# Kernel optimization log

Hardware: AMD Instinct MI355X
Metric: run time of the kernel (lower is better)

## Reference

```python
import jax, jax.numpy as jnp
import numpy as np

# Hyperparameters matching init_kwargs
DIM = 1024
HEADS = 16
MEM_HIDDEN = 512
FF_DIM = 4096
CHUNK = 128
NPERSIST = 16
ALPHA = 0.02
THETA = 0.1
ETA = 0.9
B, T = 2, 1024


def _mem_read(x, p):
    """DeepMemory forward: 2-layer MLP dim->hidden->dim with SiLU between."""
    W1, b1, W2, b2 = p
    h = jax.nn.silu(x @ W1.T + b1)
    return h @ W2.T + b2


def setup_inputs() -> dict:
    key = jax.random.key(0)
    ks = jax.random.split(key, 16)
    s = 0.02  # weight init scale
    return {
        "x": jax.random.normal(ks[0], (B, T, DIM), jnp.float32),
        "Wqkv": jax.random.normal(ks[1], (3 * DIM, DIM), jnp.float32) * s,
        "mW1": jax.random.normal(ks[2], (MEM_HIDDEN, DIM), jnp.float32) * s,
        "mb1": jnp.zeros((MEM_HIDDEN,), jnp.float32),
        "mW2": jax.random.normal(ks[3], (DIM, MEM_HIDDEN), jnp.float32) * s,
        "mb2": jnp.zeros((DIM,), jnp.float32),
        "P": jax.random.normal(ks[4], (1, NPERSIST, DIM), jnp.float32),
        "Wqkv_attn": jax.random.normal(ks[5], (3 * DIM, DIM), jnp.float32) * s,
        "Wo": jax.random.normal(ks[6], (DIM, DIM), jnp.float32) * s,
        "ffW1": jax.random.normal(ks[7], (FF_DIM, DIM), jnp.float32) * s,
        "ffb1": jnp.zeros((FF_DIM,), jnp.float32),
        "ffW2": jax.random.normal(ks[8], (DIM, FF_DIM), jnp.float32) * s,
        "ffb2": jnp.zeros((DIM,), jnp.float32),
    }


def reference(x, Wqkv, mW1, mb1, mW2, mb2, P, Wqkv_attn, Wo, ffW1, ffb1, ffW2, ffb2):
    Bb, Tt, D = x.shape
    nC = Tt // CHUNK

    # shared qkv projection (bias-free Linear)
    qkv = x @ Wqkv.T                       # [B,T,3D]
    K = qkv[..., D:2 * D]
    V = qkv[..., 2 * D:]

    # chunked test-time memory writes: k,v are detached in the torch code
    Kc = jax.lax.stop_gradient(K).reshape(Bb, nC, CHUNK, D).transpose(1, 0, 2, 3)  # [nC,B,C,D]
    Vc = jax.lax.stop_gradient(V).reshape(Bb, nC, CHUNK, D).transpose(1, 0, 2, 3)

    params0 = tuple(jax.lax.stop_gradient(p) for p in (mW1, mb1, mW2, mb2))
    mom0 = tuple(jnp.zeros_like(p) for p in params0)

    def loss_fn(p, k, v):
        return jnp.mean((_mem_read(k, p) - v) ** 2)

    def step(carry, kv):
        p, m = carry
        k, v = kv
        g = jax.grad(loss_fn)(p, k, v)
        # momentum: s = eta*s - theta*g ; weight: w = (1-alpha)*w + s
        m = tuple(ETA * mi - THETA * gi for mi, gi in zip(m, g))
        p = tuple((1.0 - ALPHA) * pi + mi for pi, mi in zip(p, m))
        return (p, m), None

    (pf, _), _ = jax.lax.scan(step, (params0, mom0), (Kc, Vc))
    pf = jax.lax.stop_gradient(pf)  # fast weights are buffers (non-differentiable)

    # memory readout tokens for the whole segment
    Q = qkv[..., :D]
    mem_tok = _mem_read(Q, pf)             # [B,T,D]

    # concatenate persistent + memory + input tokens
    tokens = jnp.concatenate([jnp.broadcast_to(P, (Bb, NPERSIST, D)), mem_tok, x], axis=1)
    N = tokens.shape[1]                    # NPERSIST + 2T
    dh = D // HEADS

    # causal multi-head attention over the concatenated sequence
    aqkv = tokens @ Wqkv_attn.T            # [B,N,3D]
    q, k, v = jnp.split(aqkv, 3, axis=-1)
    to_heads = lambda t: t.reshape(Bb, N, HEADS, dh).transpose(0, 2, 1, 3)
    q, k, v = to_heads(q), to_heads(k), to_heads(v)
    scores = jnp.einsum('bhnd,bhmd->bhnm', q, k) / jnp.sqrt(jnp.float32(dh))
    causal = jnp.tril(jnp.ones((N, N), bool))
    scores = jnp.where(causal, scores, jnp.float32(-1e9))
    attn = jax.nn.softmax(scores, axis=-1)
    o = jnp.einsum('bhnm,bhmd->bhnd', attn, v).transpose(0, 2, 1, 3).reshape(Bb, N, D)
    y = o @ Wo.T

    # feed-forward (no residual in source)
    y = jax.nn.gelu(y @ ffW1.T + ffb1) @ ffW2.T + ffb2

    # drop persistent + memory tokens, gate by a fresh memory read
    out = y[:, NPERSIST + Tt:, :]          # [B,T,D]
    newQ = (out @ Wqkv.T)[..., :D]
    return out * _mem_read(newQ, pf)
```

## Files before the change

kernel.cpp:

```cpp
#include <hip/hip_runtime.h>
#include <math.h>

#define BATCH 2
#define TSEQ 1024
#define DIMD 1024
#define NPERS 16
#define NCH 8
#define NTOK 2064
#define ETA_C 0.9f
#define THETA_C 0.1f
#define ALPHA_C 0.02f

typedef __attribute__((ext_vector_type(4))) float f32x4;
typedef __attribute__((ext_vector_type(8))) short s16x8;
typedef unsigned short u16;

__device__ __forceinline__ u16 f2bf(float f) {
    unsigned int u = __float_as_uint(f);
    return (u16)((u + 0x7fffu + ((u >> 16) & 1u)) >> 16);
}
__device__ __forceinline__ float bf2f(u16 h) { return __uint_as_float(((unsigned)h) << 16); }
__device__ __forceinline__ void split2(float v, u16& h, u16& l) {
    h = f2bf(v); l = f2bf(v - bf2f(h));
}

static const size_t oRA = 0;
static const size_t oRB = 50724864;
static const size_t oRC = 67633152;
static const size_t oRD = 80216064;
static const size_t oRE = 96993280;
static const size_t oRF = 109576192;
static const size_t oRG = 113770496;
static const size_t oRH = 117970944;

static const size_t PW1 = 0, PB1 = 524288, PW2 = 524800, PB2 = 1049088, PSZ = 1050112;

__device__ __forceinline__ void gload_lds16(const u16* g, u16* l) {
    __builtin_amdgcn_global_load_lds(
        (const __attribute__((address_space(1))) unsigned int*)g,
        (__attribute__((address_space(3))) unsigned int*)l, 16, 0, 0);
}

__device__ __forceinline__ void xcd_swizzle(int& bx, int& by) {
    int gx = gridDim.x, nwg = gx * gridDim.y;
    int lid = blockIdx.y * gx + blockIdx.x;
    int t = lid;
    if ((nwg & 7) == 0) {
        int q = nwg >> 3;
        t = (lid & 7) * q + (lid >> 3);
    }
    bx = t % gx; by = t / gx;
}

__device__ __forceinline__ void stage_tile(const u16* sp, u16* buf, int rbase,
                                           int M, int clampM, int K, int k0,
                                           int wid, int lane) {
    const int lr = lane >> 2, lc = lane & 3;
    #pragma unroll
    for (int i = 0; i < 8; ++i) {
        int r = i * 16 + lr;
        int gr = rbase + r;
        if (clampM && gr >= M) gr = M - 1;
        int g = lc ^ ((r >> 1) & 3);
        gload_lds16(sp + (size_t)gr * K + k0 + g * 8, buf + wid * 4096 + i * 512);
    }
}

__device__ __forceinline__ void stage_tile64(const u16* sp, u16* buf, int rbase,
                                             int K, int k0, int wid, int lane) {
    const int lr = lane >> 3, lc = lane & 7;
    #pragma unroll
    for (int i = 0; i < 16; ++i) {
        int r = i * 8 + lr;
        int gr = rbase + r;
        int g = lc ^ (r & 7);
        gload_lds16(sp + (size_t)gr * K + k0 + g * 8, buf + wid * 8192 + i * 512);
    }
}

template<int NPROD>
__device__ __forceinline__ void mm_loop32(u16 lds[2][16384],
                const u16* sp, int rbase, int M, int clampM, int K,
                int kbeg, int kend, int wid, int lane, int wm, int wn,
                f32x4 acc[4][4]) {
    const int frow = lane & 15, kblk = lane >> 4;
    const int nt = (kend - kbeg) >> 5;
    const int doStage = (NPROD == 3) || (wid != 1);
    if (doStage) stage_tile(sp, lds[0], rbase, M, clampM, K, kbeg, wid, lane);
    for (int t = 0; t < nt; ++t) {
        __syncthreads();
        if (t + 1 < nt && doStage)
            stage_tile(sp, lds[(t + 1) & 1], rbase, M, clampM, K, kbeg + ((t + 1) << 5), wid, lane);
        const u16* cb = lds[t & 1];
        s16x8 bh[4], bl[4];
        #pragma unroll
        for (int ni = 0; ni < 4; ++ni) {
            int br = wn * 64 + ni * 16 + frow;
            int pc = kblk ^ ((br >> 1) & 3);
            bh[ni] = *(const s16x8*)&cb[2 * 4096 + br * 32 + pc * 8];
            bl[ni] = *(const s16x8*)&cb[3 * 4096 + br * 32 + pc * 8];
        }
        #pragma unroll
        for (int mi = 0; mi < 4; ++mi) {
            int ar = wm * 64 + mi * 16 + frow;
            int pc = kblk ^ ((ar >> 1) & 3);
            s16x8 ah = *(const s16x8*)&cb[0 * 4096 + ar * 32 + pc * 8];
            s16x8 al;
            if (NPROD == 3) al = *(const s16x8*)&cb[1 * 4096 + ar * 32 + pc * 8];
            #pragma unroll
            for (int ni = 0; ni < 4; ++ni) {
                acc[mi][ni] = __builtin_amdgcn_mfma_f32_16x16x32_bf16(ah, bh[ni], acc[mi][ni], 0, 0, 0);
                acc[mi][ni] = __builtin_amdgcn_mfma_f32_16x16x32_bf16(ah, bl[ni], acc[mi][ni], 0, 0, 0);
                if (NPROD == 3)
                    acc[mi][ni] = __builtin_amdgcn_mfma_f32_16x16x32_bf16(al, bh[ni], acc[mi][ni], 0, 0, 0);
            }
        }
    }
}

template<int ACTF, int WF32, int WSPLIT, int PARTIAL, int NPROD>
__global__ __launch_bounds__(256)
void gemm_mfma_k(const u16* __restrict__ Ah, const u16* __restrict__ Al,
                 const u16* __restrict__ Wh, const u16* __restrict__ Wl,
                 float* __restrict__ C, u16* __restrict__ Chi, u16* __restrict__ Clo,
                 int M, int N, int K, const float* __restrict__ bias)
{
    __shared__ u16 lds[2][16384];
    const int tid = threadIdx.x;
    const int lane = tid & 63, wid = tid >> 6;
    const int wm = wid >> 1, wn = wid & 1;
    int bx, by; xcd_swizzle(bx, by);
    const int row0 = by * 128, col0 = bx * 128;
    const u16* sp = (wid == 0) ? Ah : (wid == 1) ? Al : (wid == 2) ? Wh : Wl;
    const int rbase = (wid < 2) ? row0 : col0;
    const int clampM = (wid < 2) ? 1 : 0;
    f32x4 acc[4][4] = {};
    int kbeg = 0, kend = K;
    if (PARTIAL) {
        int Kseg = K / gridDim.z;
        kbeg = blockIdx.z * Kseg;
        kend = kbeg + Kseg;
    }
    mm_loop32<NPROD>(lds, sp, rbase, M, clampM, K, kbeg, kend, wid, lane, wm, wn, acc);

    const int erow = (lane >> 4) * 4, ecol = lane & 15;
    #pragma unroll
    for (int mi = 0; mi < 4; ++mi) {
        #pragma unroll
        for (int ni = 0; ni < 4; ++ni) {
            int c = col0 + wn * 64 + ni * 16 + ecol;
            float bv = (!PARTIAL && bias) ? bias[c] : 0.f;
            #pragma unroll
            for (int reg = 0; reg < 4; ++reg) {
                int r = row0 + wm * 64 + mi * 16 + erow + reg;
                if (r >= M) continue;
                float v = acc[mi][ni][reg] + bv;
                if (PARTIAL) {
                    C[((size_t)blockIdx.z * M + r) * N + c] = v;
                    continue;
                }
                if (ACTF == 1) v = v / (1.f + __expf(-v));
                else if (ACTF == 2) {
                    float u = 0.7978845608028654f * (v + 0.044715f * v * v * v);
                    v = 0.5f * v * (1.f + tanhf(u));
                }
                size_t o = (size_t)r * N + c;
                if (WF32) C[o] = v;
                if (WSPLIT) { u16 h, l; split2(v, h, l); Chi[o] = h; Clo[o] = l; }
            }
        }
    }
}

__global__ __launch_bounds__(256)
void gemm_qkv_k(const u16* __restrict__ Ah, const u16* __restrict__ Al,
                const u16* __restrict__ Wh, const u16* __restrict__ Wl,
                u16* __restrict__ Qh, u16* __restrict__ Ql,
                u16* __restrict__ kch, u16* __restrict__ kcl,
                u16* __restrict__ kcTh, u16* __restrict__ kcTl,
                float* __restrict__ Vb, int M, int N, int K)
{
    __shared__ u16 lds[2][16384];
    const int tid = threadIdx.x;
    const int lane = tid & 63, wid = tid >> 6;
    const int wm = wid >> 1, wn = wid & 1;
    int bx, by; xcd_swizzle(bx, by);
    const int row0 = by * 128, col0 = bx * 128;
    const u16* sp = (wid == 0) ? Ah : (wid == 1) ? Al : (wid == 2) ? Wh : Wl;
    const int rbase = (wid < 2) ? row0 : col0;
    f32x4 acc[4][4] = {};
    mm_loop32<3>(lds, sp, rbase, M, 0, K, 0, K, wid, lane, wm, wn, acc);

    const int erow = (lane >> 4) * 4, ecol = lane & 15;
    #pragma unroll
    for (int mi = 0; mi < 4; ++mi) {
        #pragma unroll
        for (int ni = 0; ni < 4; ++ni) {
            int c = col0 + wn * 64 + ni * 16 + ecol;
            #pragma unroll
            for (int reg = 0; reg < 4; ++reg) {
                int r = row0 + wm * 64 + mi * 16 + erow + reg;
                float v = acc[mi][ni][reg];
                int b = r >> 10, t = r & 1023;
                if (c < 1024) {
                    size_t o = (size_t)r * 1024 + c;
                    u16 h, l; split2(v, h, l); Qh[o] = h; Ql[o] = l;
                } else if (c < 2048) {
                    int d = c - 1024;
                    int ch = t >> 7, rr = t & 127;
                    size_t o = ((size_t)((ch * 2 + b) * 128 + rr)) * 1024 + d;
                    u16 h, l; split2(v, h, l);
                    kch[o] = h; kcl[o] = l;
                    size_t ot = (size_t)ch * 262144 + (size_t)d * 256 + b * 128 + rr;
                    kcTh[ot] = h; kcTl[ot] = l;
                } else {
                    int d = c - 2048;
                    int ch = t >> 7, rr = t & 127;
                    Vb[((size_t)((ch * 2 + b) * 128 + rr)) * 1024 + d] = v;
                }
            }
        }
    }
}

__global__ __launch_bounds__(256)
void gemm_aqkv_k(const u16* __restrict__ Ah, const u16* __restrict__ Al,
                 const u16* __restrict__ Wh, const u16* __restrict__ Wl,
                 u16* __restrict__ fQh, u16* __restrict__ fQl,
                 u16* __restrict__ fKh, u16* __restrict__ fKl,
                 u16* __restrict__ fVt, int M, int N, int K)
{
    __shared__ u16 lds[2][16384];
    const int tid = threadIdx.x;
    const int lane = tid & 63, wid = tid >> 6;
    const int wm = wid >> 1, wn = wid & 1;
    int bx, by; xcd_swizzle(bx, by);
    if (bx < 8 && ((by <= 7) || (by >= 17 && by <= 23))) return;
    const int row0 = by * 128, col0 = bx * 128;
    const u16* sp = (wid == 0) ? Ah : (wid == 1) ? Al : (wid == 2) ? Wh : Wl;
    const int rbase = (wid < 2) ? row0 : col0;
    const int clampM = (wid < 2) ? 1 : 0;
    f32x4 acc[4][4] = {};
    mm_loop32<2>(lds, sp, rbase, M, clampM, K, 0, K, wid, lane, wm, wn, acc);

    const int erow = (lane >> 4) * 4, ecol = lane & 15;
    #pragma unroll
    for (int mi = 0; mi < 4; ++mi) {
        #pragma unroll
        for (int ni = 0; ni < 4; ++ni) {
            int c = col0 + wn * 64 + ni * 16 + ecol;
            #pragma unroll
            for (int reg = 0; reg < 4; ++reg) {
                int r = row0 + wm * 64 + mi * 16 + erow + reg;
                if (r >= M) continue;
                float v = acc[mi][ni][reg];
                int b = (r >= 2064) ? 1 : 0;
                int n = r - b * 2064;
                if (c < 1024) {
                    if (n >= NPERS + TSEQ) {
                        int h = c >> 6, d = c & 63;
                        int row = n - (NPERS + TSEQ);
                        size_t o = (((size_t)(b * 16 + h)) * 1024 + row) * 64 + d;
                        u16 hh, ll; split2(0.125f * v, hh, ll);
                        fQh[o] = hh; fQl[o] = ll;
                    }
                } else if (c < 2048) {
                    int cc = c - 1024;
                    int h = cc >> 6, d = cc & 63;
                    size_t o = (((size_t)(b * 16 + h)) * NTOK + n) * 64 + d;
                    u16 hh, ll; split2(v, hh, ll);
                    fKh[o] = hh; fKl[o] = ll;
                } else {
                    int cc = c - 2048;
                    int h = cc >> 6, d = cc & 63;
                    fVt[(((size_t)(b * 16 + h)) * 64 + d) * NTOK + n] = f2bf(v);
                }
            }
        }
    }
}

template<int ACTF, int WF32, int WSPLIT>
__global__ __launch_bounds__(256)
void reduce_k(const float* __restrict__ Cp, int S,
              float* __restrict__ C, u16* __restrict__ Chi, u16* __restrict__ Clo,
              const float* __restrict__ bias, int M, int N)
{
    int i = blockIdx.x * 256 + threadIdx.x;
    int n4 = (int)((size_t)M * N / 4);
    if (i >= n4) return;
    size_t off = (size_t)i * 4;
    float4 v = *(const float4*)&Cp[off];
    for (int z = 1; z < S; ++z) {
        float4 u = *(const float4*)&Cp[(size_t)z * M * N + off];
        v.x += u.x; v.y += u.y; v.z += u.z; v.w += u.w;
    }
    int c = (int)(off % N);
    float vv[4] = {v.x, v.y, v.z, v.w};
    #pragma unroll
    for (int j = 0; j < 4; ++j) {
        float w = vv[j];
        if (bias) w += bias[c + j];
        if (ACTF == 1) w = w / (1.f + __expf(-w));
        else if (ACTF == 2) {
            float u = 0.7978845608028654f * (w + 0.044715f * w * w * w);
            w = 0.5f * w * (1.f + tanhf(u));
        }
        if (WF32) C[off + j] = w;
        if (WSPLIT) { u16 h, l; split2(w, h, l); Chi[off + j] = h; Clo[off + j] = l; }
    }
}

__global__ __launch_bounds__(256)
void reduce_tok_k(const float* __restrict__ Cp, const float* __restrict__ bias,
                  u16* __restrict__ th, u16* __restrict__ tl)
{
    int i = blockIdx.x * 256 + threadIdx.x;
    if (i >= 524288) return;
    size_t off = (size_t)i * 4;
    float4 v = *(const float4*)&Cp[off];
    float4 u = *(const float4*)&Cp[2097152 + off];
    v.x += u.x; v.y += u.y; v.z += u.z; v.w += u.w;
    int r = (int)(off >> 10), c = (int)(off & 1023);
    int b = r >> 10, t = r & 1023;
    size_t orow = (((size_t)(b * NTOK + NPERS + t)) << 10) + c;
    float vv[4] = {v.x + bias[c], v.y + bias[c + 1], v.z + bias[c + 2], v.w + bias[c + 3]};
    u16 h0,l0,h1,l1,h2,l2,h3,l3;
    split2(vv[0],h0,l0); split2(vv[1],h1,l1); split2(vv[2],h2,l2); split2(vv[3],h3,l3);
    ushort4 hv = {h0,h1,h2,h3}, lv = {l0,l1,l2,l3};
    *(ushort4*)&th[orow] = hv;
    *(ushort4*)&tl[orow] = lv;
}

static void gemm_mfma(hipStream_t s, int act, int wf32, int wsplit,
                      const u16* Ah, const u16* Al, const u16* Wh, const u16* Wl,
                      float* C, u16* Ch, u16* Cl, int M, int N, int K,
                      const float* bias, int nprod = 3)
{
    dim3 g(N / 128, (M + 127) / 128), b(256);
    if (act == 0 && wf32 == 1 && wsplit == 0)
        gemm_mfma_k<0,1,0,0,3><<<g,b,0,s>>>(Ah,Al,Wh,Wl,C,Ch,Cl,M,N,K,bias);
    else if (act == 0 && wf32 == 1 && wsplit == 1)
        gemm_mfma_k<0,1,1,0,3><<<g,b,0,s>>>(Ah,Al,Wh,Wl,C,Ch,Cl,M,N,K,bias);
    else if (act == 0 && wf32 == 0 && wsplit == 1)
        gemm_mfma_k<0,0,1,0,3><<<g,b,0,s>>>(Ah,Al,Wh,Wl,C,Ch,Cl,M,N,K,bias);
    else if (act == 1)
        gemm_mfma_k<1,0,1,0,3><<<g,b,0,s>>>(Ah,Al,Wh,Wl,C,Ch,Cl,M,N,K,bias);
    else if (nprod == 2)
        gemm_mfma_k<2,0,1,0,2><<<g,b,0,s>>>(Ah,Al,Wh,Wl,C,Ch,Cl,M,N,K,bias);
    else
        gemm_mfma_k<2,0,1,0,3><<<g,b,0,s>>>(Ah,Al,Wh,Wl,C,Ch,Cl,M,N,K,bias);
}

static void gemm_mfma_sk(hipStream_t s, int act, int wf32, int wsplit,
                         const u16* Ah, const u16* Al, const u16* Wh, const u16* Wl,
                         float* C, u16* Ch, u16* Cl, int M, int N, int K,
                         const float* bias, int S, float* part, int nprod = 3)
{
    if (S <= 1) { gemm_mfma(s, act, wf32, wsplit, Ah, Al, Wh, Wl, C, Ch, Cl, M, N, K, bias, nprod); return; }
    dim3 g(N / 128, (M + 127) / 128, S), b(256);
    if (nprod == 2)
        gemm_mfma_k<0,0,0,1,2><<<g,b,0,s>>>(Ah,Al,Wh,Wl,part,nullptr,nullptr,M,N,K,nullptr);
    else
        gemm_mfma_k<0,0,0,1,3><<<g,b,0,s>>>(Ah,Al,Wh,Wl,part,nullptr,nullptr,M,N,K,nullptr);
    int n4 = (int)((size_t)M * N / 4);
    dim3 rg((n4 + 255) / 256), rb(256);
    if (act == 0 && wf32 == 1 && wsplit == 0)
        reduce_k<0,1,0><<<rg,rb,0,s>>>(part, S, C, Ch, Cl, bias, M, N);
    else if (act == 0 && wf32 == 1 && wsplit == 1)
        reduce_k<0,1,1><<<rg,rb,0,s>>>(part, S, C, Ch, Cl, bias, M, N);
    else if (act == 0 && wf32 == 0 && wsplit == 1)
        reduce_k<0,0,1><<<rg,rb,0,s>>>(part, S, C, Ch, Cl, bias, M, N);
    else if (act == 1)
        reduce_k<1,0,1><<<rg,rb,0,s>>>(part, S, C, Ch, Cl, bias, M, N);
    else
        reduce_k<2,0,1><<<rg,rb,0,s>>>(part, S, C, Ch, Cl, bias, M, N);
}

template<int MODE>
__device__ __forceinline__ void scan_body(u16* lds, int bx, int by,
                 const u16* __restrict__ Ah, const u16* __restrict__ Al,
                 const u16* __restrict__ Wh, const u16* __restrict__ Wl,
                 float* __restrict__ C, u16* __restrict__ Chi, u16* __restrict__ Clo,
                 u16* __restrict__ ChiT, u16* __restrict__ CloT,
                 const float* __restrict__ Zf, const float* __restrict__ add,
                 const float* __restrict__ bias, float* __restrict__ CP,
                 int M, int N, int K, float alpha)
{
    const int tid = threadIdx.x;
    const int lane = tid & 63, wid = tid >> 6;
    const int wm = wid >> 1, wn = wid & 1;
    const int row0 = by * 128, col0 = bx * 128;

    const u16* sp = (wid == 0) ? Ah : (wid == 1) ? Al : (wid == 2) ? Wh : Wl;
    const int rbase = (wid < 2) ? row0 : col0;

    f32x4 acc[4][4] = {};
    const int frow = lane & 15, kblk = lane >> 4;
    const int nt = K >> 6;

    stage_tile64(sp, lds, rbase, K, 0, wid, lane);

    for (int t = 0; t < nt; ++t) {
        __syncthreads();
        if (t + 1 < nt)
            stage_tile64(sp, lds + (((t + 1) & 1) << 15), rbase, K, (t + 1) << 6, wid, lane);
        const u16* cb = lds + ((t & 1) << 15);

        #pragma unroll
        for (int s = 0; s < 2; ++s) {
            s16x8 bh[4], bl[4];
            #pragma unroll
            for (int ni = 0; ni < 4; ++ni) {
                int br = wn * 64 + ni * 16 + frow;
                int pc = (s * 4 + kblk) ^ (br & 7);
                bh[ni] = *(const s16x8*)&cb[2 * 8192 + br * 64 + pc * 8];
                bl[ni] = *(const s16x8*)&cb[3 * 8192 + br * 64 + pc * 8];
            }
            #pragma unroll
            for (int mi = 0; mi < 4; ++mi) {
                int ar = wm * 64 + mi * 16 + frow;
                int pc = (s * 4 + kblk) ^ (ar & 7);
                s16x8 ah = *(const s16x8*)&cb[0 * 8192 + ar * 64 + pc * 8];
                s16x8 al = *(const s16x8*)&cb[1 * 8192 + ar * 64 + pc * 8];
                #pragma unroll
                for (int ni = 0; ni < 4; ++ni) {
                    acc[mi][ni] = __builtin_amdgcn_mfma_f32_16x16x32_bf16(ah, bh[ni], acc[mi][ni], 0, 0, 0);
                    acc[mi][ni] = __builtin_amdgcn_mfma_f32_16x16x32_bf16(ah, bl[ni], acc[mi][ni], 0, 0, 0);
                    acc[mi][ni] = __builtin_amdgcn_mfma_f32_16x16x32_bf16(al, bh[ni], acc[mi][ni], 0, 0, 0);
                }
            }
        }
    }

    const int erow = (lane >> 4) * 4, ecol = lane & 15;
    float csum[4] = {0.f, 0.f, 0.f, 0.f};
    #pragma unroll
    for (int mi = 0; mi < 4; ++mi) {
        #pragma unroll
        for (int ni = 0; ni < 4; ++ni) {
            int c = col0 + wn * 64 + ni * 16 + ecol;
            #pragma unroll
            for (int reg = 0; reg < 4; ++reg) {
                int r = row0 + wm * 64 + mi * 16 + erow + reg;
                float v = acc[mi][ni][reg];
                size_t o = (size_t)r * N + c;
                if (MODE == 1) {
                    v += bias[c];
                    C[o] = v;
                    float hv = v / (1.f + __expf(-v));
                    u16 h, l; split2(hv, h, l);
                    Chi[o] = h; Clo[o] = l;
                    size_t ot = (size_t)c * M + r;
                    ChiT[ot] = h; CloT[ot] = l;
                } else if (MODE == 2) {
                    v += bias[c] - add[o];
                    u16 h, l; split2(v, h, l);
                    Chi[o] = h; Clo[o] = l;
                    size_t ot = (size_t)c * M + r;
                    ChiT[ot] = h; CloT[ot] = l;
                    csum[ni] += v;
                } else if (MODE == 3) {
                    C[o] = alpha * v;
                } else {
                    v *= alpha;
                    float z = Zf[o];
                    float sg = 1.f / (1.f + __expf(-z));
                    v *= sg * (1.f + z * (1.f - sg));
                    u16 h, l; split2(v, h, l);
                    size_t ot = (size_t)c * M + r;
                    ChiT[ot] = h; CloT[ot] = l;
                    csum[ni] += v;
                }
            }
        }
    }
    if (MODE == 2 || MODE == 4) {
        #pragma unroll
        for (int ni = 0; ni < 4; ++ni) {
            float s = csum[ni];
            s += __shfl_xor(s, 16);
            s += __shfl_xor(s, 32);
            if ((lane >> 4) == 0) {
                int c = col0 + wn * 64 + ni * 16 + ecol;
                float w = (MODE == 2) ? alpha * s : s;
                CP[(size_t)(by * 2 + wm) * N + c] = w;
            }
        }
    }
}

template<int MODE>
__global__ __launch_bounds__(256)
void gemm_scan_k(const u16* __restrict__ Ah, const u16* __restrict__ Al,
                 const u16* __restrict__ Wh, const u16* __restrict__ Wl,
                 float* __restrict__ C, u16* __restrict__ Chi, u16* __restrict__ Clo,
                 u16* __restrict__ ChiT, u16* __restrict__ CloT,
                 const float* __restrict__ Zf, const float* __restrict__ add,
                 const float* __restrict__ bias, float* __restrict__ CP,
                 int M, int N, int K, float alpha)
{
    __shared__ u16 lds[2][32768];
    int bx, by; xcd_swizzle(bx, by);
    scan_body<MODE>(&lds[0][0], bx, by, Ah, Al, Wh, Wl, C, Chi, Clo, ChiT, CloT,
                    Zf, add, bias, CP, M, N, K, alpha);
}

__global__ __launch_bounds__(256)
void gemm_scan_pair_k(const u16* __restrict__ rTh, const u16* __restrict__ rTl,
                      const u16* __restrict__ hTh, const u16* __restrict__ hTl,
                      float* __restrict__ gW2,
                      const u16* __restrict__ rh_, const u16* __restrict__ rl_,
                      const u16* __restrict__ w2th, const u16* __restrict__ w2tl,
                      u16* __restrict__ dhTh, u16* __restrict__ dhTl,
                      const float* __restrict__ z1, float* __restrict__ cp1, float cs)
{
    __shared__ u16 lds[2][32768];
    if (blockIdx.y < 8) {
        scan_body<3>(&lds[0][0], blockIdx.x, blockIdx.y, rTh, rTl, hTh, hTl,
                     gW2, nullptr, nullptr, nullptr, nullptr, nullptr, nullptr,
                     nullptr, nullptr, 1024, 512, 256, cs);
    } else {
        scan_body<4>(&lds[0][0], blockIdx.x, blockIdx.y - 8, rh_, rl_, w2th, w2tl,
                     nullptr, nullptr, nullptr, dhTh, dhTl, z1, nullptr,
                     nullptr, cp1, 256, 512, 1024, cs);
    }
}

__global__ void cvt_split_k(const float* __restrict__ in, u16* __restrict__ hi,
                            u16* __restrict__ lo, int n4) {
    int i = blockIdx.x * 256 + threadIdx.x;
    if (i >= n4) return;
    float4 v = *(const float4*)&in[(size_t)i * 4];
    u16 h0,l0,h1,l1,h2,l2,h3,l3;
    split2(v.x,h0,l0); split2(v.y,h1,l1); split2(v.z,h2,l2); split2(v.w,h3,l3);
    ushort4 hv = {h0,h1,h2,h3}, lv = {l0,l1,l2,l3};
    *(ushort4*)&hi[(size_t)i * 4] = hv;
    *(ushort4*)&lo[(size_t)i * 4] = lv;
}
__global__ void transpose_split_k(const float* __restrict__ in, u16* __restrict__ outh,
                                  u16* __restrict__ outl, int R, int C) {
    __shared__ float t[32][33];
    const int c0 = blockIdx.x * 32, r0 = blockIdx.y * 32;
    const size_t zoff = (size_t)blockIdx.z * R * C;
    const int tx = threadIdx.x & 31, ty = threadIdx.x >> 5;
    #pragma unroll
    for (int p = 0; p < 4; ++p) {
        int r = ty + p * 8;
        t[r][tx] = in[zoff + (size_t)(r0 + r) * C + c0 + tx];
    }
    __syncthreads();
    #pragma unroll
    for (int p = 0; p < 4; ++p) {
        int cc = ty + p * 8;
        float v = t[tx][cc];
        u16 h, l; split2(v, h, l);
        size_t o = zoff + (size_t)(c0 + cc) * R + r0 + tx;
        outh[o] = h; outl[o] = l;
    }
}
__global__ void update3_k(float* __restrict__ p, float* __restrict__ mo,
                          const float* __restrict__ g,
                          const float* __restrict__ cp1, const float* __restrict__ cp2,
                          u16* __restrict__ w1h, u16* __restrict__ w1l,
                          u16* __restrict__ w2h, u16* __restrict__ w2l,
                          u16* __restrict__ w2th, u16* __restrict__ w2tl, int n) {
    int i = blockIdx.x * 256 + threadIdx.x;
    if (i >= n) return;
    float gi;
    if (i < 524288) gi = g[i];
    else if (i < 524800) {
        int j = i - 524288;
        gi = cp1[j] + cp1[512 + j] + cp1[1024 + j] + cp1[1536 + j];
    } else if (i < 1049088) gi = g[i];
    else {
        int j = i - 1049088;
        gi = cp2[j] + cp2[1024 + j] + cp2[2048 + j] + cp2[3072 + j];
    }
    float m = ETA_C * mo[i] - THETA_C * gi;
    mo[i] = m;
    float pv = (1.f - ALPHA_C) * p[i] + m;
    p[i] = pv;
    if (i < 524288) {
        u16 h, l; split2(pv, h, l); w1h[i] = h; w1l[i] = l;
    } else if (i >= 524800 && i < 1049088) {
        int j = i - 524800;
        u16 h, l; split2(pv, h, l);
        w2h[j] = h; w2l[j] = l;
        int tj = (j & 511) * 1024 + (j >> 9);
        w2th[tj] = h; w2tl[tj] = l;
    }
}
__global__ void tokens_px_k(const float* __restrict__ P, const float* __restrict__ x,
                            u16* __restrict__ th, u16* __restrict__ tl) {
    size_t idx = (size_t)blockIdx.x * 256 + threadIdx.x;
    if (idx >= (size_t)2 * 1040 * 1024) return;
    int d = (int)(idx & 1023);
    int rl = (int)((idx >> 10) % 1040);
    int b = (int)(idx / ((size_t)1040 * 1024));
    float v; int n;
    if (rl < NPERS) { v = P[(size_t)rl * 1024 + d]; n = rl; }
    else { int t = rl - NPERS; v = x[((size_t)b * TSEQ + t) * 1024 + d]; n = NPERS + TSEQ + t; }
    size_t o = (((size_t)(b * NTOK + n)) << 10) + d;
    u16 h, l; split2(v, h, l); th[o] = h; tl[o] = l;
}
__global__ void mul_k(const float* __restrict__ a, const float* __restrict__ b,
                      float* __restrict__ o, int n) {
    int i = blockIdx.x * 256 + threadIdx.x;
    if (i < n) o[i] = a[i] * b[i];
}

__global__ __launch_bounds__(256)
void flash_part_k(const u16* __restrict__ Qsh, const u16* __restrict__ Qsl,
                  const u16* __restrict__ Ksh, const u16* __restrict__ Ksl,
                  const u16* __restrict__ Vts, float* __restrict__ Of,
                  float* __restrict__ Lf)
{
    __shared__ u16 lds[20480];
    u16* KH = lds;            u16* KL = lds + 4096;
    u16* VT = lds + 8192;
    u16* PH = lds + 12288;    u16* PL = lds + 16384;

    int lid = blockIdx.x + (blockIdx.y << 4) + (blockIdx.z << 8);
    int t1024 = ((lid & 7) << 7) | (lid >> 3);
    const int qt = t1024 & 15, h = (t1024 >> 4) & 15;
    const int zb = t1024 >> 8;
    const int b = zb >> 1, z = zb & 1;

    const int tid = threadIdx.x;
    const int lane = tid & 63, wid = tid >> 6;
    const int fr = lane & 15, kq = lane >> 4;
    const int bh = b * 16 + h;
    const int q0c = qt * 64;
    const int q0a = NPERS + TSEQ + q0c;
    const int ntile = ((q0a + 63) >> 6) + 1;
    const int half = ntile >> 1;
    const int jt0 = z ? half : 0;
    const int jt1 = z ? ntile : half;
    const int l8 = lane & 7, lr8 = lane >> 3;

    auto stageKV = [&](int jt) {
        const int j0 = jt * 64;
        #pragma unroll
        for (int jj = 0; jj < 6; ++jj) {
            int j = wid * 6 + jj;
            int buf = j >> 3, i8 = j & 7;
            if (buf < 2) {
                int row = i8 * 8 + lr8;
                int grow = j0 + row; if (grow > NTOK - 1) grow = NTOK - 1;
                int c = l8 ^ (row & 7);
                const u16* src = (buf == 0 ? Ksh : Ksl) +
                                 (((size_t)bh * NTOK + grow) << 6) + c * 8;
                gload_lds16(src, (buf == 0 ? KH : KL) + i8 * 512);
            } else {
                int d = i8 * 8 + lr8;
                int c = l8 ^ (d & 7);
                int col = j0 + c * 8; if (col > NTOK - 8) col = NTOK - 8;
                const u16* src = Vts + ((size_t)bh * 64 + d) * NTOK + col;
                gload_lds16(src, VT + i8 * 512);
            }
        }
    };

    s16x8 qh[2], ql[2];
    {
        const size_t qrow = ((size_t)bh * 1024 + q0c + wid * 16 + fr) << 6;
        #pragma unroll
        for (int kb = 0; kb < 2; ++kb) {
            qh[kb] = *(const s16x8*)&Qsh[qrow + (size_t)(kb * 4 + kq) * 8];
            ql[kb] = *(const s16x8*)&Qsl[qrow + (size_t)(kb * 4 + kq) * 8];
        }
    }

    f32x4 Oa[4] = {};
    float lrow[4] = {0.f, 0.f, 0.f, 0.f};

    for (int jt = jt0; jt < jt1; ++jt) {
        const int j0 = jt * 64;
        stageKV(jt);
        __syncthreads();

        f32x4 sacc[4] = {};
        __builtin_amdgcn_s_setprio(1);
        #pragma unroll
        for (int nt = 0; nt < 4; ++nt) {
            #pragma unroll
            for (int kb = 0; kb < 2; ++kb) {
                int br = nt * 16 + fr;
                int sl = (kb * 4 + kq) ^ (fr & 7);
                s16x8 kh = *(const s16x8*)&KH[br * 64 + sl * 8];
                s16x8 kl = *(const s16x8*)&KL[br * 64 + sl * 8];
                sacc[nt] = __builtin_amdgcn_mfma_f32_16x16x32_bf16(qh[kb], kh, sacc[nt], 0, 0, 0);
                sacc[nt] = __builtin_amdgcn_mfma_f32_16x16x32_bf16(ql[kb], kh, sacc[nt], 0, 0, 0);
                sacc[nt] = __builtin_amdgcn_mfma_f32_16x16x32_bf16(qh[kb], kl, sacc[nt], 0, 0, 0);
            }
        }
        __builtin_amdgcn_s_setprio(0);

        #pragma unroll
        for (int r = 0; r < 4; ++r) {
            const int qloc = kq * 4 + r;
            const int qi = q0a + wid * 16 + qloc;
            float p4[4], psum = 0.f;
            #pragma unroll
            for (int nt = 0; nt < 4; ++nt) {
                int kj = j0 + nt * 16 + fr;
                float e = (kj <= qi) ? __expf(sacc[nt][r]) : 0.f;
                p4[nt] = e; psum += e;
            }
            #pragma unroll
            for (int off = 1; off < 16; off <<= 1)
                psum += __shfl_xor(psum, off);
            lrow[r] += psum;
            const int prow = wid * 16 + qloc;
            #pragma unroll
            for (int nt = 0; nt < 4; ++nt) {
                u16 ph, pl; split2(p4[nt], ph, pl);
                int col = nt * 16 + fr;
                int sl = (col >> 3) ^ (qloc & 7);
                int off = prow * 64 + sl * 8 + (col & 7);
                PH[off] = ph; PL[off] = pl;
            }
        }

        __builtin_amdgcn_s_setprio(1);
        #pragma unroll
        for (int kb = 0; kb < 2; ++kb) {
            int pr = wid * 16 + fr;
            int sl = (kb * 4 + kq) ^ (fr & 7);
            s16x8 pa = *(const s16x8*)&PH[pr * 64 + sl * 8];
            s16x8 pb = *(const s16x8*)&PL[pr * 64 + sl * 8];
            #pragma unroll
            for (int dt = 0; dt < 4; ++dt) {
                int vr = dt * 16 + fr;
                s16x8 vb = *(const s16x8*)&VT[vr * 64 + sl * 8];
                Oa[dt] = __builtin_amdgcn_mfma_f32_16x16x32_bf16(pa, vb, Oa[dt], 0, 0, 0);
                Oa[dt] = __builtin_amdgcn_mfma_f32_16x16x32_bf16(pb, vb, Oa[dt], 0, 0, 0);
            }
        }
        __builtin_amdgcn_s_setprio(0);
        __syncthreads();
    }

    const size_t obase = ((((size_t)z * 2 + b) * 16 + h) * 16 + qt) * 4096;
    const size_t mlb   = ((((size_t)z * 2 + b) * 16 + h) * 16 + qt) * 64;
    #pragma unroll
    for (int r = 0; r < 4; ++r) {
        int rl = wid * 16 + kq * 4 + r;
        if (fr == 0) Lf[mlb + rl] = lrow[r];
        #pragma unroll
        for (int dt = 0; dt < 4; ++dt)
            Of[obase + (size_t)rl * 64 + dt * 16 + fr] = Oa[dt][r];
    }
}

__global__ __launch_bounds__(256)
void flash_merge_k(const float* __restrict__ Of, const float* __restrict__ Lf,
                   u16* __restrict__ oh, u16* __restrict__ ol)
{
    const int qt = blockIdx.x, h = blockIdx.y, b = blockIdx.z;
    const int tid = threadIdx.x;
    const int row = tid >> 2, quad = tid & 3;
    const size_t b0 = ((((size_t)0 * 2 + b) * 16 + h) * 16 + qt) * 4096 + (size_t)row * 64;
    const size_t b1 = ((((size_t)1 * 2 + b) * 16 + h) * 16 + qt) * 4096 + (size_t)row * 64;
    const size_t m0i = ((((size_t)0 * 2 + b) * 16 + h) * 16 + qt) * 64 + row;
    const size_t m1i = ((((size_t)1 * 2 + b) * 16 + h) * 16 + qt) * 64 + row;
    float inv = 1.f / (Lf[m0i] + Lf[m1i]);
    const size_t orow = ((size_t)(b * 1024 + qt * 64 + row)) * 1024 + h * 64;
    #pragma unroll
    for (int i = 0; i < 4; ++i) {
        int col = quad * 16 + i * 4;
        float4 v0 = *(const float4*)&Of[b0 + col];
        float4 v1 = *(const float4*)&Of[b1 + col];
        float o0 = (v0.x + v1.x) * inv;
        float o1 = (v0.y + v1.y) * inv;
        float o2 = (v0.z + v1.z) * inv;
        float o3 = (v0.w + v1.w) * inv;
        u16 h0,l0_,h1,l1_,h2,l2_,h3,l3_;
        split2(o0,h0,l0_); split2(o1,h1,l1_); split2(o2,h2,l2_); split2(o3,h3,l3_);
        ushort4 hv = {h0,h1,h2,h3}, lv = {l0_,l1_,l2_,l3_};
        *(ushort4*)&oh[orow + col] = hv;
        *(ushort4*)&ol[orow + col] = lv;
    }
}

extern "C" void kernel_launch(void* const* d_in, const int* in_sizes, int n_in,
                              void* d_out, int out_size, void* d_ws, size_t ws_size,
                              hipStream_t stream)
{
    const float* x     = (const float*)d_in[0];
    const float* Wqkv  = (const float*)d_in[1];
    const float* mW1   = (const float*)d_in[2];
    const float* mb1   = (const float*)d_in[3];
    const float* mW2   = (const float*)d_in[4];
    const float* mb2   = (const float*)d_in[5];
    const float* Pp    = (const float*)d_in[6];
    const float* Wqa   = (const float*)d_in[7];
    const float* Wo    = (const float*)d_in[8];
    const float* ffW1  = (const float*)d_in[9];
    const float* ffb1  = (const float*)d_in[10];
    const float* ffW2  = (const float*)d_in[11];
    const float* ffb2  = (const float*)d_in[12];
    char* wsb = (char*)d_ws;
    float* outp = (float*)d_out;

    float* z1    = (float*)(wsb + oRA);
    float* grd   = (float*)(wsb + oRA + 3145728);
    float* cp2   = (float*)(wsb + oRA + 7346176);
    float* cp1   = (float*)(wsb + oRA + 7362560);
    u16* hh_     = (u16*)(wsb + oRA + 8388608);
    u16* hl_     = (u16*)(wsb + oRA + 8650752);
    u16* hTh     = (u16*)(wsb + oRA + 9437184);
    u16* hTl     = (u16*)(wsb + oRA + 9699328);
    u16* rh_     = (u16*)(wsb + oRA + 10485760);
    u16* rl_     = (u16*)(wsb + oRA + 11010048);
    u16* rTh     = (u16*)(wsb + oRA + 11534336);
    u16* rTl     = (u16*)(wsb + oRA + 12058624);
    u16* dhTh    = (u16*)(wsb + oRA + 12582912);
    u16* dhTl    = (u16*)(wsb + oRA + 12845056);
    u16* kcTh    = (u16*)(wsb + oRA + 16777216);
    u16* kcTl    = (u16*)(wsb + oRA + 20971520);
    float* Of    = (float*)(wsb + oRA);
    float* Lf    = (float*)(wsb + oRA + 16777216);
    u16* fVth    = (u16*)(wsb + oRA + 17825792);
    u16* fKl     = (u16*)(wsb + oRA + 26279936);
    u16* Woh     = (u16*)(wsb + oRA);
    u16* Wol     = (u16*)(wsb + oRA + 2097152);
    u16* ffhh    = (u16*)(wsb + oRA);
    u16* ffhl    = (u16*)(wsb + oRA + 16777216);
    u16* outbh   = (u16*)(wsb + oRA + 33554432);
    u16* outbl   = (u16*)(wsb + oRA + 37748736);
    u16* newQh   = (u16*)(wsb + oRA);
    u16* newQl   = (u16*)(wsb + oRA + 4194304);
    u16* hzh     = (u16*)(wsb + oRA + 8388608);
    u16* hzl     = (u16*)(wsb + oRA + 10485760);
    float* memq  = (float*)(wsb + oRA + 12582912);
    float* partA0 = (float*)(wsb + oRA);
    float* partA1 = (float*)(wsb + oRA + 4194304);
    float* partA2 = (float*)(wsb + oRA + 16777216);
    float* Vb    = (float*)(wsb + oRB + 8388608);
    u16* tokh    = (u16*)(wsb + oRB);
    u16* tokl    = (u16*)(wsb + oRB + 8454144);
    u16* oh      = (u16*)(wsb + oRB);
    u16* ol      = (u16*)(wsb + oRB + 4194304);
    u16* y1h     = (u16*)(wsb + oRB + 8388608);
    u16* y1l     = (u16*)(wsb + oRB + 12582912);
    float* partB = (float*)(wsb + oRB);
    u16* xh      = (u16*)(wsb + oRC);
    u16* xl      = (u16*)(wsb + oRC + 4194304);
    float* mom   = (float*)(wsb + oRC);
    u16* pW2Th   = (u16*)(wsb + oRC + 5242880);
    u16* pW2Tl   = (u16*)(wsb + oRC + 6291456);
    u16* Wqah    = (u16*)(wsb + oRC);
    u16* Wqal    = (u16*)(wsb + oRC + 6291456);
    u16* Qh      = (u16*)(wsb + oRD);
    u16* Ql      = (u16*)(wsb + oRD + 4194304);
    u16* kchh    = (u16*)(wsb + oRD + 8388608);
    u16* kchl    = (u16*)(wsb + oRD + 12582912);
    u16* t1h     = (u16*)(wsb + oRD + 8388608);
    u16* t1l     = (u16*)(wsb + oRD + 10485760);
    u16* fKh     = (u16*)(wsb + oRD);
    u16* ffW1h   = (u16*)(wsb + oRD);
    u16* ffW1l   = (u16*)(wsb + oRD + 8388608);
    u16* ffW2h   = (u16*)(wsb + oRD);
    u16* ffW2l   = (u16*)(wsb + oRD + 8388608);
    u16* Wqkvh   = (u16*)(wsb + oRE);
    u16* Wqkvl   = (u16*)(wsb + oRE + 6291456);
    u16* pW1h    = (u16*)(wsb + oRF);
    u16* pW1l    = (u16*)(wsb + oRF + 1048576);
    u16* pW2h    = (u16*)(wsb + oRF + 2097152);
    u16* pW2l    = (u16*)(wsb + oRF + 3145728);
    float* par   = (float*)(wsb + oRG);
    float* outb  = (float*)(wsb + oRH);
    u16* fQh     = (u16*)(wsb + oRH);
    u16* fQl     = (u16*)(wsb + oRH + 4194304);

    hipMemcpyAsync(par + PW1, mW1, 524288 * sizeof(float), hipMemcpyDeviceToDevice, stream);
    hipMemcpyAsync(par + PB1, mb1, 512 * sizeof(float), hipMemcpyDeviceToDevice, stream);
    hipMemcpyAsync(par + PW2, mW2, 524288 * sizeof(float), hipMemcpyDeviceToDevice, stream);
    hipMemcpyAsync(par + PB2, mb2, 1024 * sizeof(float), hipMemcpyDeviceToDevice, stream);

    cvt_split_k<<<2048, 256, 0, stream>>>(x, xh, xl, 524288);
    cvt_split_k<<<3072, 256, 0, stream>>>(Wqkv, Wqkvh, Wqkvl, 786432);
    gemm_qkv_k<<<dim3(24, 16), 256, 0, stream>>>(xh, xl, Wqkvh, Wqkvl,
        Qh, Ql, kchh, kchl, kcTh, kcTl, Vb, 2048, 3072, 1024);

    hipMemsetAsync(mom, 0, PSZ * sizeof(float), stream);
    cvt_split_k<<<512, 256, 0, stream>>>(par + PW1, pW1h, pW1l, 131072);
    cvt_split_k<<<512, 256, 0, stream>>>(par + PW2, pW2h, pW2l, 131072);
    transpose_split_k<<<dim3(16, 32, 1), 256, 0, stream>>>(par + PW2, pW2Th, pW2Tl, 1024, 512);

    const float cs = 2.f / (float)(BATCH * 128 * DIMD);
    for (int c = 0; c < NCH; ++c) {
        const u16* kch = kchh + (size_t)c * 262144;
        const u16* kcl = kchl + (size_t)c * 262144;
        const u16* kth = kcTh + (size_t)c * 262144;
        const u16* ktl = kcTl + (size_t)c * 262144;
        const float* vc = Vb + (size_t)c * 262144;
        gemm_scan_k<1><<<dim3(4, 2), 256, 0, stream>>>(kch, kcl, pW1h, pW1l,
            z1, hh_, hl_, hTh, hTl, nullptr, nullptr, par + PB1, nullptr, 256, 512, 1024, 1.f);
        gemm_scan_k<2><<<dim3(8, 2), 256, 0, stream>>>(hh_, hl_, pW2h, pW2l,
            nullptr, rh_, rl_, rTh, rTl, nullptr, vc, par + PB2, cp2, 256, 1024, 512, cs);
        gemm_scan_pair_k<<<dim3(4, 10), 256, 0, stream>>>(rTh, rTl, hTh, hTl, grd + PW2,
            rh_, rl_, pW2Th, pW2Tl, dhTh, dhTl, z1, cp1, cs);
        gemm_scan_k<3><<<dim3(8, 4), 256, 0, stream>>>(dhTh, dhTl, kth, ktl,
            grd + PW1, nullptr, nullptr, nullptr, nullptr, nullptr, nullptr, nullptr, nullptr,
            512, 1024, 256, 1.f);
        update3_k<<<4102, 256, 0, stream>>>(par, mom, grd, cp1, cp2,
            pW1h, pW1l, pW2h, pW2l, pW2Th, pW2Tl, (int)PSZ);
    }

    gemm_mfma_sk(stream, 1, 0, 1, Qh, Ql, pW1h, pW1l, nullptr, t1h, t1l,
                 2048, 512, 1024, par + PB1, 4, partA2);
    {
        dim3 g(8, 16, 2), b(256);
        gemm_mfma_k<0,0,0,1,3><<<g, b, 0, stream>>>(t1h, t1l, pW2h, pW2l,
            partA0, nullptr, nullptr, 2048, 1024, 512, nullptr);
        reduce_tok_k<<<2048, 256, 0, stream>>>(partA0, par + PB2, tokh, tokl);
    }

    tokens_px_k<<<8320, 256, 0, stream>>>(Pp, x, tokh, tokl);
    cvt_split_k<<<3072, 256, 0, stream>>>(Wqa, Wqah, Wqal, 786432);
    gemm_aqkv_k<<<dim3(24, 33), 256, 0, stream>>>(tokh, tokl, Wqah, Wqal,
        fQh, fQl, fKh, fKl, fVth, 4128, 3072, 1024);

    flash_part_k<<<dim3(16, 16, 4), 256, 0, stream>>>(fQh, fQl, fKh, fKl, fVth, Of, Lf);
    flash_merge_k<<<dim3(16, 16, 2), 256, 0, stream>>>(Of, Lf, oh, ol);

    cvt_split_k<<<1024, 256, 0, stream>>>(Wo, Woh, Wol, 262144);
    gemm_mfma_sk(stream, 0, 0, 1, oh, ol, Woh, Wol, nullptr, y1h, y1l,
                 2048, 1024, 1024, nullptr, 2, partA1);
    cvt_split_k<<<4096, 256, 0, stream>>>(ffW1, ffW1h, ffW1l, 1048576);
    gemm_mfma(stream, 2, 0, 1, y1h, y1l, ffW1h, ffW1l, nullptr, ffhh, ffhl,
              2048, 4096, 1024, ffb1, 2);
    cvt_split_k<<<4096, 256, 0, stream>>>(ffW2, ffW2h, ffW2l, 1048576);
    gemm_mfma_sk(stream, 0, 1, 1, ffhh, ffhl, ffW2h, ffW2l, outb, outbh, outbl,
                 2048, 1024, 4096, ffb2, 2, partB, 2);

    gemm_mfma_sk(stream, 0, 0, 1, outbh, outbl, Wqkvh, Wqkvl, nullptr, newQh, newQl,
                 2048, 1024, 1024, nullptr, 2, partB);
    gemm_mfma_sk(stream, 1, 0, 1, newQh, newQl, pW1h, pW1l, nullptr, hzh, hzl,
                 2048, 512, 1024, par + PB1, 4, partB);
    gemm_mfma_sk(stream, 0, 1, 0, hzh, hzl, pW2h, pW2l, memq, nullptr, nullptr,
                 2048, 1024, 512, par + PB2, 2, partB);
    mul_k<<<8192, 256, 0, stream>>>(outb, memq, outp, 2097152);
}
```

Before: 1.335 ms.

## Drop third split-bf16 product in several GEMMs and add column-major tile swizzle

Several GEMMs (memory read of Q, Wo projection, newQ projection, hidden layer of the final memory read) now use two bf16 MFMA products (hi*hi + hi*lo) instead of three, dropping the lo*hi correction term. This cuts MFMA work on those GEMMs by a third at the cost of some accuracy. Separately, a column-major block-index mapping option is added to the XCD swizzle and enabled for the QKV and attention-QKV GEMMs and the FF1 GEMM, to improve weight-tile L2 reuse across co-scheduled workgroups. The last memory GEMM is explicitly kept at three products.

```diff
diff --git a/kernel.cpp b/kernel.cpp
--- a/kernel.cpp
+++ b/kernel.cpp
@@ -41,16 +41,18 @@
         (__attribute__((address_space(3))) unsigned int*)l, 16, 0, 0);
 }
 
-__device__ __forceinline__ void xcd_swizzle(int& bx, int& by) {
-    int gx = gridDim.x, nwg = gx * gridDim.y;
-    int lid = blockIdx.y * gx + blockIdx.x;
+__device__ __forceinline__ void xcd_swz2(int cmaj, int& bx, int& by) {
+    int gx = gridDim.x, gy = gridDim.y, nwg = gx * gy;
+    int lid = cmaj ? (blockIdx.x * gy + blockIdx.y) : (blockIdx.y * gx + blockIdx.x);
     int t = lid;
     if ((nwg & 7) == 0) {
         int q = nwg >> 3;
         t = (lid & 7) * q + (lid >> 3);
     }
-    bx = t % gx; by = t / gx;
-}
+    if (cmaj) { by = t % gy; bx = t / gy; }
+    else      { bx = t % gx; by = t / gx; }
+}
+__device__ __forceinline__ void xcd_swizzle(int& bx, int& by) { xcd_swz2(0, bx, by); }
 
 __device__ __forceinline__ void stage_tile(const u16* sp, u16* buf, int rbase,
                                            int M, int clampM, int K, int k0,
@@ -123,13 +125,13 @@
 void gemm_mfma_k(const u16* __restrict__ Ah, const u16* __restrict__ Al,
                  const u16* __restrict__ Wh, const u16* __restrict__ Wl,
                  float* __restrict__ C, u16* __restrict__ Chi, u16* __restrict__ Clo,
-                 int M, int N, int K, const float* __restrict__ bias)
+                 int M, int N, int K, const float* __restrict__ bias, int cmaj)
 {
     __shared__ u16 lds[2][16384];
     const int tid = threadIdx.x;
     const int lane = tid & 63, wid = tid >> 6;
     const int wm = wid >> 1, wn = wid & 1;
-    int bx, by; xcd_swizzle(bx, by);
+    int bx, by; xcd_swz2(cmaj, bx, by);
     const int row0 = by * 128, col0 = bx * 128;
     const u16* sp = (wid == 0) ? Ah : (wid == 1) ? Al : (wid == 2) ? Wh : Wl;
     const int rbase = (wid < 2) ? row0 : col0;
@@ -184,7 +186,7 @@
     const int tid = threadIdx.x;
     const int lane = tid & 63, wid = tid >> 6;
     const int wm = wid >> 1, wn = wid & 1;
-    int bx, by; xcd_swizzle(bx, by);
+    int bx, by; xcd_swz2(1, bx, by);
     const int row0 = by * 128, col0 = bx * 128;
     const u16* sp = (wid == 0) ? Ah : (wid == 1) ? Al : (wid == 2) ? Wh : Wl;
     const int rbase = (wid < 2) ? row0 : col0;
@@ -234,7 +236,7 @@
     const int tid = threadIdx.x;
     const int lane = tid & 63, wid = tid >> 6;
     const int wm = wid >> 1, wn = wid & 1;
-    int bx, by; xcd_swizzle(bx, by);
+    int bx, by; xcd_swz2(1, bx, by);
     if (bx < 8 && ((by <= 7) || (by >= 17 && by <= 23))) return;
     const int row0 = by * 128, col0 = bx * 128;
     const u16* sp = (wid == 0) ? Ah : (wid == 1) ? Al : (wid == 2) ? Wh : Wl;
@@ -335,34 +337,35 @@
 static void gemm_mfma(hipStream_t s, int act, int wf32, int wsplit,
                       const u16* Ah, const u16* Al, const u16* Wh, const u16* Wl,
                       float* C, u16* Ch, u16* Cl, int M, int N, int K,
-                      const float* bias, int nprod = 3)
+                      const float* bias, int nprod = 3, int cmaj = 0)
 {
     dim3 g(N / 128, (M + 127) / 128), b(256);
     if (act == 0 && wf32 == 1 && wsplit == 0)
-        gemm_mfma_k<0,1,0,0,3><<<g,b,0,s>>>(Ah,Al,Wh,Wl,C,Ch,Cl,M,N,K,bias);
+        gemm_mfma_k<0,1,0,0,3><<<g,b,0,s>>>(Ah,Al,Wh,Wl,C,Ch,Cl,M,N,K,bias,cmaj);
     else if (act == 0 && wf32 == 1 && wsplit == 1)
-        gemm_mfma_k<0,1,1,0,3><<<g,b,0,s>>>(Ah,Al,Wh,Wl,C,Ch,Cl,M,N,K,bias);
+        gemm_mfma_k<0,1,1,0,3><<<g,b,0,s>>>(Ah,Al,Wh,Wl,C,Ch,Cl,M,N,K,bias,cmaj);
     else if (act == 0 && wf32 == 0 && wsplit == 1)
-        gemm_mfma_k<0,0,1,0,3><<<g,b,0,s>>>(Ah,Al,Wh,Wl,C,Ch,Cl,M,N,K,bias);
+        gemm_mfma_k<0,0,1,0,3><<<g,b,0,s>>>(Ah,Al,Wh,Wl,C,Ch,Cl,M,N,K,bias,cmaj);
     else if (act == 1)
-        gemm_mfma_k<1,0,1,0,3><<<g,b,0,s>>>(Ah,Al,Wh,Wl,C,Ch,Cl,M,N,K,bias);
+        gemm_mfma_k<1,0,1,0,3><<<g,b,0,s>>>(Ah,Al,Wh,Wl,C,Ch,Cl,M,N,K,bias,cmaj);
     else if (nprod == 2)
-        gemm_mfma_k<2,0,1,0,2><<<g,b,0,s>>>(Ah,Al,Wh,Wl,C,Ch,Cl,M,N,K,bias);
+        gemm_mfma_k<2,0,1,0,2><<<g,b,0,s>>>(Ah,Al,Wh,Wl,C,Ch,Cl,M,N,K,bias,cmaj);
     else
-        gemm_mfma_k<2,0,1,0,3><<<g,b,0,s>>>(Ah,Al,Wh,Wl,C,Ch,Cl,M,N,K,bias);
+        gemm_mfma_k<2,0,1,0,3><<<g,b,0,s>>>(Ah,Al,Wh,Wl,C,Ch,Cl,M,N,K,bias,cmaj);
 }
 
 static void gemm_mfma_sk(hipStream_t s, int act, int wf32, int wsplit,
                          const u16* Ah, const u16* Al, const u16* Wh, const u16* Wl,
                          float* C, u16* Ch, u16* Cl, int M, int N, int K,
-                         const float* bias, int S, float* part, int nprod = 3)
-{
-    if (S <= 1) { gemm_mfma(s, act, wf32, wsplit, Ah, Al, Wh, Wl, C, Ch, Cl, M, N, K, bias, nprod); return; }
+                         const float* bias, int S, float* part, int nprod = 3,
+                         int cmaj = 0)
+{
+    if (S <= 1) { gemm_mfma(s, act, wf32, wsplit, Ah, Al, Wh, Wl, C, Ch, Cl, M, N, K, bias, nprod, cmaj); return; }
     dim3 g(N / 128, (M + 127) / 128, S), b(256);
     if (nprod == 2)
-        gemm_mfma_k<0,0,0,1,2><<<g,b,0,s>>>(Ah,Al,Wh,Wl,part,nullptr,nullptr,M,N,K,nullptr);
+        gemm_mfma_k<0,0,0,1,2><<<g,b,0,s>>>(Ah,Al,Wh,Wl,part,nullptr,nullptr,M,N,K,nullptr,cmaj);
     else
-        gemm_mfma_k<0,0,0,1,3><<<g,b,0,s>>>(Ah,Al,Wh,Wl,part,nullptr,nullptr,M,N,K,nullptr);
+        gemm_mfma_k<0,0,0,1,3><<<g,b,0,s>>>(Ah,Al,Wh,Wl,part,nullptr,nullptr,M,N,K,nullptr,cmaj);
     int n4 = (int)((size_t)M * N / 4);
     dim3 rg((n4 + 255) / 256), rb(256);
     if (act == 0 && wf32 == 1 && wsplit == 0)
@@ -911,11 +914,11 @@
     }
 
     gemm_mfma_sk(stream, 1, 0, 1, Qh, Ql, pW1h, pW1l, nullptr, t1h, t1l,
-                 2048, 512, 1024, par + PB1, 4, partA2);
+                 2048, 512, 1024, par + PB1, 4, partA2, 2);
     {
         dim3 g(8, 16, 2), b(256);
-        gemm_mfma_k<0,0,0,1,3><<<g, b, 0, stream>>>(t1h, t1l, pW2h, pW2l,
-            partA0, nullptr, nullptr, 2048, 1024, 512, nullptr);
+        gemm_mfma_k<0,0,0,1,2><<<g, b, 0, stream>>>(t1h, t1l, pW2h, pW2l,
+            partA0, nullptr, nullptr, 2048, 1024, 512, nullptr, 0);
         reduce_tok_k<<<2048, 256, 0, stream>>>(partA0, par + PB2, tokh, tokl);
     }
 
@@ -929,19 +932,19 @@
 
     cvt_split_k<<<1024, 256, 0, stream>>>(Wo, Woh, Wol, 262144);
     gemm_mfma_sk(stream, 0, 0, 1, oh, ol, Woh, Wol, nullptr, y1h, y1l,
-                 2048, 1024, 1024, nullptr, 2, partA1);
+                 2048, 1024, 1024, nullptr, 2, partA1, 2);
     cvt_split_k<<<4096, 256, 0, stream>>>(ffW1, ffW1h, ffW1l, 1048576);
     gemm_mfma(stream, 2, 0, 1, y1h, y1l, ffW1h, ffW1l, nullptr, ffhh, ffhl,
-              2048, 4096, 1024, ffb1, 2);
+              2048, 4096, 1024, ffb1, 2, 1);
     cvt_split_k<<<4096, 256, 0, stream>>>(ffW2, ffW2h, ffW2l, 1048576);
     gemm_mfma_sk(stream, 0, 1, 1, ffhh, ffhl, ffW2h, ffW2l, outb, outbh, outbl,
                  2048, 1024, 4096, ffb2, 2, partB, 2);
 
     gemm_mfma_sk(stream, 0, 0, 1, outbh, outbl, Wqkvh, Wqkvl, nullptr, newQh, newQl,
-                 2048, 1024, 1024, nullptr, 2, partB);
+                 2048, 1024, 1024, nullptr, 2, partB, 2);
     gemm_mfma_sk(stream, 1, 0, 1, newQh, newQl, pW1h, pW1l, nullptr, hzh, hzl,
-                 2048, 512, 1024, par + PB1, 4, partB);
+                 2048, 512, 1024, par + PB1, 4, partB, 2);
     gemm_mfma_sk(stream, 0, 1, 0, hzh, hzl, pW2h, pW2l, memq, nullptr, nullptr,
-                 2048, 1024, 512, par + PB2, 2, partB);
+                 2048, 1024, 512, par + PB2, 2, partB, 3);
     mul_k<<<8192, 256, 0, stream>>>(outb, memq, outp, 2097152);
 }
```

Result: no change. 1.333 ms (median of 2 runs) (-0.2%).
